# Optimization experiments

Measured on AMD Instinct MI355X. Metric: run time of the kernel, lower is better.

## Reference

```python
import jax, jax.numpy as jnp
import numpy as np

N_NODES = 50000
N_EDGES = 800000
IN_CH = 128
HID = 128
OUT_CH = 16
N_LAYERS = 3
N_GRAPHS = 128
BN_EPS = 1e-5


def setup_inputs() -> dict:
    key = jax.random.key(0)
    ks = jax.random.split(key, 12)
    x = jax.random.normal(ks[0], (N_NODES, IN_CH), dtype=jnp.float32)
    edge_index = jax.random.randint(ks[1], (2, N_EDGES), 0, N_NODES, dtype=jnp.int64)
    batch = jnp.sort(jax.random.randint(ks[2], (N_NODES,), 0, N_GRAPHS, dtype=jnp.int64))
    s = 1.0 / np.sqrt(HID)
    W1 = jax.random.normal(ks[3], (N_LAYERS, IN_CH, HID), dtype=jnp.float32) * s
    b1 = jax.random.normal(ks[4], (N_LAYERS, HID), dtype=jnp.float32) * s
    W2 = jax.random.normal(ks[5], (N_LAYERS, HID, HID), dtype=jnp.float32) * s
    b2 = jax.random.normal(ks[6], (N_LAYERS, HID), dtype=jnp.float32) * s
    gamma = jnp.ones((N_LAYERS, HID), dtype=jnp.float32)
    beta = jnp.zeros((N_LAYERS, HID), dtype=jnp.float32)
    mean = jax.random.normal(ks[7], (N_LAYERS, HID), dtype=jnp.float32) * 0.1
    var = jax.random.uniform(ks[8], (N_LAYERS, HID), dtype=jnp.float32, minval=0.5, maxval=1.5)
    Wc = jax.random.normal(ks[9], (HID, OUT_CH), dtype=jnp.float32) * s
    bc = jax.random.normal(ks[10], (OUT_CH,), dtype=jnp.float32) * s
    return {"x": x, "edge_index": edge_index, "batch": batch, "W1": W1, "b1": b1,
            "W2": W2, "b2": b2, "gamma": gamma, "beta": beta, "mean": mean,
            "var": var, "Wc": Wc, "bc": bc}


def reference(x, edge_index, batch, W1, b1, W2, b2, gamma, beta, mean, var, Wc, bc):
    # GIN (eval mode: BN uses running stats, dropout is identity).
    src, dst = edge_index[0], edge_index[1]
    n = x.shape[0]
    h = x
    for i in range(N_LAYERS):
        # GINConv with eps=0: MLP(x + sum_{j->i} x_j)
        agg = jax.ops.segment_sum(h[src], dst, num_segments=n)  # [N, d]
        z = h + agg
        z = jnp.maximum(z @ W1[i] + b1[i], 0.0) @ W2[i] + b2[i]  # 2-layer MLP
        # BatchNorm1d (eval) + ReLU
        inv = gamma[i] * jax.lax.rsqrt(var[i] + BN_EPS)
        h = jnp.maximum((z - mean[i]) * inv + beta[i], 0.0)
    pooled = jax.ops.segment_sum(h, batch, num_segments=N_GRAPHS)  # [G, hid]
    return pooled @ Wc + bc
```

## Files before the change

### kernel.cpp

```cpp
#include <hip/hip_runtime.h>

#define N_NODES 50000
#define N_EDGES 800000
#define CH 128
#define N_GRAPHS 128
#define N_LAYERS 3
#define OUT_CH 16
#define BN_EPS 1e-5f
#define ZN N_NODES
#define NB 196
#define BCAP 4608
#define PBCAP 8448
#define EPB 4096
#define NTILES (N_NODES / 16)
#define SSTRIDE 20
#define BINB 196
#define CB 6250
#define PB 388

typedef unsigned short ushort_t;
typedef __attribute__((ext_vector_type(8))) short bf16x8;
typedef __attribute__((ext_vector_type(8))) unsigned short u16x8;
typedef __attribute__((ext_vector_type(4))) float f32x4;

__device__ inline ushort_t f2b(float f) {
    unsigned u = __float_as_uint(f);
    unsigned r = (u + 0x7fffu + ((u >> 16) & 1u)) >> 16;
    return (ushort_t)r;
}
__device__ inline float blo(unsigned u) { return __uint_as_float(u << 16); }
__device__ inline float bhi(unsigned u) { return __uint_as_float(u & 0xffff0000u); }

__global__ __launch_bounds__(256) void setup_bin_kernel(
    const int* __restrict__ src, const int* __restrict__ dst,
    int* __restrict__ gcur, unsigned* __restrict__ gbuck,
    const float4* __restrict__ x, ushort4* __restrict__ xb, ushort4* __restrict__ xz,
    float* __restrict__ pooled,
    const float* __restrict__ W1, const float* __restrict__ W2, ushort_t* __restrict__ Wt,
    const float* __restrict__ b1, const float* __restrict__ b2,
    const float* __restrict__ gamma, const float* __restrict__ beta,
    const float* __restrict__ mean, const float* __restrict__ var,
    float* __restrict__ scale, float* __restrict__ shift) {
    int bid = blockIdx.x, t = threadIdx.x;
    if (bid < BINB) {
        __shared__ int lcnt[256];
        __shared__ int lpref[256];
        __shared__ int lpos[NB];
        __shared__ int lbase[NB];
        __shared__ unsigned stage[EPB];
        __shared__ unsigned char sbk[EPB];
        int e0 = bid * EPB;
        int nloc = N_EDGES - e0; if (nloc > EPB) nloc = EPB;

        lcnt[t] = 0;
        __syncthreads();

        int2 ed[16];
        const int4* s4 = (const int4*)(src + e0);
        const int4* d4 = (const int4*)(dst + e0);
        #pragma unroll
        for (int k = 0; k < 4; ++k) {
            int base = k * 1024 + t * 4;
            if (base + 3 < nloc) {
                int4 sv = s4[k * 256 + t];
                int4 dv = d4[k * 256 + t];
                ed[k * 4 + 0].x = sv.x; ed[k * 4 + 0].y = dv.x;
                ed[k * 4 + 1].x = sv.y; ed[k * 4 + 1].y = dv.y;
                ed[k * 4 + 2].x = sv.z; ed[k * 4 + 2].y = dv.z;
                ed[k * 4 + 3].x = sv.w; ed[k * 4 + 3].y = dv.w;
            } else {
                #pragma unroll
                for (int m = 0; m < 4; ++m) {
                    int i = base + m;
                    if (i < nloc) {
                        ed[k * 4 + m].x = src[e0 + i];
                        ed[k * 4 + m].y = dst[e0 + i];
                    } else ed[k * 4 + m].y = -1;
                }
            }
        }
        #pragma unroll
        for (int j = 0; j < 16; ++j)
            if (ed[j].y >= 0) atomicAdd(&lcnt[ed[j].y >> 8], 1);
        __syncthreads();
        int v = lcnt[t];
        lpref[t] = v;
        __syncthreads();
        for (int off = 1; off < 256; off <<= 1) {
            int y = (t >= off) ? lpref[t - off] : 0;
            __syncthreads();
            lpref[t] += y;
            __syncthreads();
        }
        int excl = lpref[t] - v;
        __syncthreads();
        lpref[t] = excl;
        if (t < NB) {
            lpos[t] = excl;
            lbase[t] = atomicAdd(&gcur[t], v);
        }
        __syncthreads();
        #pragma unroll
        for (int j = 0; j < 16; ++j) {
            if (ed[j].y >= 0) {
                int b = ed[j].y >> 8;
                int slot = atomicAdd(&lpos[b], 1);
                stage[slot] = (unsigned)ed[j].x | ((unsigned)(ed[j].y & 255) << 16);
                sbk[slot] = (unsigned char)b;
            }
        }
        __syncthreads();
        for (int i = t; i < nloc; i += 256) {
            int b = sbk[i];
            gbuck[(size_t)b * BCAP + lbase[b] + (i - lpref[b])] = stage[i];
        }
    } else if (bid < BINB + CB) {
        int i = (bid - BINB) * 256 + t;
        if (i < N_GRAPHS * CH) pooled[i] = 0.f;
        if (bid == BINB && t < 32) {
            ushort4 zz; zz.x = 0; zz.y = 0; zz.z = 0; zz.w = 0;
            xb[(size_t)ZN * 32 + t] = zz;
            xz[(size_t)ZN * 32 + t] = zz;
        }
        float4 v = x[i];
        ushort4 o;
        o.x = f2b(v.x); o.y = f2b(v.y); o.z = f2b(v.z); o.w = f2b(v.w);
        xb[i] = o;
    } else {
        int i = (bid - BINB - CB) * 256 + t;
        if (i < 6 * CH * CH) {
            int mat = i >> 14, r = i & 16383;
            int j = r & 7, bb = r >> 3;
            int lane = bb & 63, cs = bb >> 6;
            int ct = cs >> 2, ks = cs & 3;
            int n = ct * 16 + (lane & 15);
            int k = ks * 32 + (lane >> 4) * 8 + j;
            const float* Wsrc = (mat < 3) ? (W1 + (size_t)mat * CH * CH)
                                          : (W2 + (size_t)(mat - 3) * CH * CH);
            Wt[i] = f2b(Wsrc[k * CH + n]);
        } else {
            int e = i - 6 * CH * CH;
            if (e >= 6 * CH) return;
            int mat = e / CH, c = e % CH;
            if (mat < 3) {
                scale[e] = 1.f;
                shift[e] = b1[mat * CH + c];
            } else {
                int l = mat - 3;
                float inv = gamma[l * CH + c] * rsqrtf(var[l * CH + c] + BN_EPS);
                scale[e] = inv;
                shift[e] = (b2[l * CH + c] - mean[l * CH + c]) * inv + beta[l * CH + c];
            }
        }
    }
}

__global__ __launch_bounds__(256) void place_kernel(const int* __restrict__ gcur,
                                                    const unsigned* __restrict__ gbuck,
                                                    int* __restrict__ rowptr,
                                                    ushort_t* __restrict__ esrc) {
    __shared__ ushort_t ssrc[BCAP];
    __shared__ unsigned char sd[BCAP];
    __shared__ ushort_t outS[PBCAP];
    __shared__ int cnt[256], pref[256], cur[256];
    int b = blockIdx.x, t = threadIdx.x;
    cnt[t] = 0;
    __syncthreads();
    int nb = gcur[b];
    for (int i = t; i < nb; i += 256) {
        unsigned p = gbuck[(size_t)b * BCAP + i];
        ssrc[i] = (ushort_t)(p & 0xffffu);
        int dl = (p >> 16) & 0xff;
        sd[i] = (unsigned char)dl;
        atomicAdd(&cnt[dl], 1);
    }
    __syncthreads();
    int v = cnt[t];
    int pc = (v + 15) & ~15;
    pref[t] = pc;
    __syncthreads();
    for (int off = 1; off < 256; off <<= 1) {
        int y = (t >= off) ? pref[t - off] : 0;
        __syncthreads();
        pref[t] += y;
        __syncthreads();
    }
    int excl = pref[t] - pc;
    int total = pref[255];
    __syncthreads();
    pref[t] = excl;
    cur[t] = 0;
    int idx = (b << 8) + t;
    if (idx < N_NODES)
        rowptr[idx] = (b * PBCAP + excl) | ((pc >> 4) << 24);
    __syncthreads();
    for (int i = t; i < total; i += 256) outS[i] = (ushort_t)ZN;
    __syncthreads();
    for (int i = t; i < nb; i += 256) {
        int dl = sd[i];
        int p = pref[dl] + atomicAdd(&cur[dl], 1);
        outS[p] = ssrc[i];
    }
    __syncthreads();
    for (int i = t; i < total; i += 256)
        esrc[(size_t)b * PBCAP + i] = outS[i];
}

__global__ __launch_bounds__(512, 8) void layer_kernel(
    const unsigned* __restrict__ h2, const int* __restrict__ rowptr,
    const ushort_t* __restrict__ esrc,
    const ushort_t* __restrict__ Wf1, const ushort_t* __restrict__ Wf2,
    const float* __restrict__ shift1, const float* __restrict__ scale2,
    const float* __restrict__ shift2, ushort_t* __restrict__ hout,
    const int* __restrict__ batch, float* __restrict__ pooled, int do_pool) {
    __shared__ unsigned zt[16][68];
    __shared__ ushort_t sS[CH * SSTRIDE];

    int t = threadIdx.x;
    int wave = t >> 6, lane = t & 63;
    int quad = lane >> 4, l16 = lane & 15;
    int row0 = blockIdx.x * 16;

    {
        int node0 = row0 + wave * 2;
        unsigned self0 = h2[(size_t)node0 * 64 + lane];
        unsigned self1 = h2[(size_t)(node0 + 1) * 64 + lane];
        int pr0 = __builtin_amdgcn_readfirstlane(rowptr[node0]);
        int pr1 = __builtin_amdgcn_readfirstlane(rowptr[node0 + 1]);
        int e  = pr0 & 0xFFFFFF;
        int rA = (int)((unsigned)pr0 >> 24);
        int rounds = rA + (int)((unsigned)pr1 >> 24);
        float ax = blo(self0), ay = bhi(self0);
        float sx = 0.f, sy = 0.f;
        unsigned ucur[16];
        if (rounds > 0) {
            u16x8 i0 = *(const u16x8*)(esrc + e);
            u16x8 i1 = *(const u16x8*)(esrc + e + 8);
            #pragma unroll
            for (int j = 0; j < 8; ++j) ucur[j] = h2[(size_t)i0[j] * 64 + lane];
            #pragma unroll
            for (int j = 0; j < 8; ++j) ucur[8 + j] = h2[(size_t)i1[j] * 64 + lane];
        }
        for (int r = 0; r < rounds; ++r) {
            unsigned un[16];
            if (r + 1 < rounds) {
                const ushort_t* ep = esrc + e + 16;
                u16x8 i0 = *(const u16x8*)ep;
                u16x8 i1 = *(const u16x8*)(ep + 8);
                #pragma unroll
                for (int j = 0; j < 8; ++j) un[j] = h2[(size_t)i0[j] * 64 + lane];
                #pragma unroll
                for (int j = 0; j < 8; ++j) un[8 + j] = h2[(size_t)i1[j] * 64 + lane];
            }
            if (r == rA) { sx = ax; sy = ay; ax = blo(self1); ay = bhi(self1); }
            #pragma unroll
            for (int j = 0; j < 16; ++j) { ax += blo(ucur[j]); ay += bhi(ucur[j]); }
            if (r + 1 < rounds) {
                #pragma unroll
                for (int j = 0; j < 16; ++j) ucur[j] = un[j];
            }
            e += 16;
        }
        float bx, by;
        if (rA == rounds) {
            sx = ax; sy = ay;
            bx = blo(self1); by = bhi(self1);
        } else {
            bx = ax; by = ay;
        }
        zt[wave * 2][lane]     = ((unsigned)f2b(sy) << 16) | (unsigned)f2b(sx);
        zt[wave * 2 + 1][lane] = ((unsigned)f2b(by) << 16) | (unsigned)f2b(bx);
    }
    __syncthreads();

    {
        bf16x8 af[4];
        #pragma unroll
        for (int ks = 0; ks < 4; ++ks)
            af[ks] = *(const bf16x8*)((const ushort_t*)&zt[l16][0] + ks * 32 + quad * 8);
        bf16x8 w1[4];
        #pragma unroll
        for (int ks = 0; ks < 4; ++ks)
            w1[ks] = *(const bf16x8*)(Wf1 + ((size_t)(wave * 4 + ks) * 64 + lane) * 8);
        f32x4 acc = (f32x4){0.f, 0.f, 0.f, 0.f};
        #pragma unroll
        for (int ks = 0; ks < 4; ++ks)
            acc = __builtin_amdgcn_mfma_f32_16x16x32_bf16(af[ks], w1[ks], acc, 0, 0, 0);
        int k = wave * 16 + l16;
        float sh = shift1[k];
        uint2 p;
        p.x = ((unsigned)f2b(fmaxf(acc[1] + sh, 0.f)) << 16)
            |  (unsigned)f2b(fmaxf(acc[0] + sh, 0.f));
        p.y = ((unsigned)f2b(fmaxf(acc[3] + sh, 0.f)) << 16)
            |  (unsigned)f2b(fmaxf(acc[2] + sh, 0.f));
        *(uint2*)&sS[k * SSTRIDE + quad * 4] = p;
    }
    __syncthreads();

    {
        bf16x8 af2[4];
        #pragma unroll
        for (int ks = 0; ks < 4; ++ks)
            #pragma unroll
            for (int j = 0; j < 8; ++j)
                af2[ks][j] = (short)sS[(ks * 32 + quad * 8 + j) * SSTRIDE + l16];
        bf16x8 w2[4];
        #pragma unroll
        for (int ks = 0; ks < 4; ++ks)
            w2[ks] = *(const bf16x8*)(Wf2 + ((size_t)(wave * 4 + ks) * 64 + lane) * 8);
        f32x4 acc = (f32x4){0.f, 0.f, 0.f, 0.f};
        #pragma unroll
        for (int ks = 0; ks < 4; ++ks)
            acc = __builtin_amdgcn_mfma_f32_16x16x32_bf16(af2[ks], w2[ks], acc, 0, 0, 0);
        int col = wave * 16 + l16;
        float sc = scale2[col], sh = shift2[col];
        float hv[4];
        #pragma unroll
        for (int r = 0; r < 4; ++r)
            hv[r] = fmaxf(acc[r] * sc + sh, 0.f);
        if (!do_pool) {
            #pragma unroll
            for (int r = 0; r < 4; ++r) {
                int row = row0 + quad * 4 + r;
                hout[(size_t)row * CH + col] = f2b(hv[r]);
            }
        } else {
            int g0 = batch[row0], g15 = batch[row0 + 15];
            if (g0 == g15) {
                float s = hv[0] + hv[1] + hv[2] + hv[3];
                s += __shfl_xor(s, 16);
                s += __shfl_xor(s, 32);
                if (quad == 0) atomicAdd(&pooled[g0 * CH + col], s);
            } else {
                #pragma unroll
                for (int r = 0; r < 4; ++r) {
                    int row = row0 + quad * 4 + r;
                    atomicAdd(&pooled[batch[row] * CH + col], hv[r]);
                }
            }
        }
    }
}

__global__ __launch_bounds__(256) void cls_kernel(const float* __restrict__ pooled,
                                                  const float* __restrict__ Wc,
                                                  const float* __restrict__ bc,
                                                  float* __restrict__ out) {
    int i = blockIdx.x * blockDim.x + threadIdx.x;
    if (i >= N_GRAPHS * OUT_CH) return;
    int g = i / OUT_CH, o = i % OUT_CH;
    float s = bc[o];
    for (int k = 0; k < CH; ++k) s += pooled[g * CH + k] * Wc[k * OUT_CH + o];
    out[i] = s;
}

extern "C" void kernel_launch(void* const* d_in, const int* in_sizes, int n_in,
                              void* d_out, int out_size, void* d_ws, size_t ws_size,
                              hipStream_t stream) {
    const float* x     = (const float*)d_in[0];
    const int*   eidx  = (const int*)d_in[1];
    const int*   batch = (const int*)d_in[2];
    const float* W1    = (const float*)d_in[3];
    const float* b1    = (const float*)d_in[4];
    const float* W2    = (const float*)d_in[5];
    const float* b2    = (const float*)d_in[6];
    const float* gamma = (const float*)d_in[7];
    const float* beta  = (const float*)d_in[8];
    const float* mean  = (const float*)d_in[9];
    const float* var   = (const float*)d_in[10];
    const float* Wc    = (const float*)d_in[11];
    const float* bc    = (const float*)d_in[12];
    float* out = (float*)d_out;

    const int* src = eidx;
    const int* dst = eidx + N_EDGES;

    char* w = (char*)d_ws;
    size_t off = 0;
    auto alloc = [&](size_t bytes) { void* p = w + off; off += (bytes + 255) & ~(size_t)255; return p; };
    int*      gcur   = (int*)alloc(NB * 4);
    unsigned* gbuck  = (unsigned*)alloc((size_t)NB * BCAP * 4);
    int*      rowptr = (int*)alloc(N_NODES * 4);
    ushort_t* esrc   = (ushort_t*)alloc((size_t)NB * PBCAP * 2);
    ushort_t* Bh     = (ushort_t*)alloc((size_t)(N_NODES + 1) * CH * 2);
    ushort_t* Bz     = (ushort_t*)alloc((size_t)(N_NODES + 1) * CH * 2);
    ushort_t* Wt     = (ushort_t*)alloc((size_t)6 * CH * CH * 2);
    float*    scale  = (float*)alloc(6 * CH * 4);
    float*    shift  = (float*)alloc(6 * CH * 4);
    float*    pooled = (float*)alloc(N_GRAPHS * CH * 4);
    (void)ws_size; (void)n_in; (void)in_sizes; (void)out_size;

    hipMemsetAsync(gcur, 0, NB * 4, stream);
    setup_bin_kernel<<<BINB + CB + PB, 256, 0, stream>>>(
        src, dst, gcur, gbuck,
        (const float4*)x, (ushort4*)Bh, (ushort4*)Bz, pooled,
        W1, W2, Wt, b1, b2, gamma, beta, mean, var, scale, shift);
    place_kernel<<<NB, 256, 0, stream>>>(gcur, gbuck, rowptr, esrc);

    ushort_t* bufA = Bh;
    ushort_t* bufB = Bz;
    for (int i = 0; i < N_LAYERS; ++i) {
        int last = (i == N_LAYERS - 1);
        layer_kernel<<<NTILES, 512, 0, stream>>>((const unsigned*)bufA, rowptr, esrc,
                                                 Wt + (size_t)i * CH * CH,
                                                 Wt + (size_t)(3 + i) * CH * CH,
                                                 shift + i * CH,
                                                 scale + (3 + i) * CH,
                                                 shift + (3 + i) * CH,
                                                 bufB, batch, pooled, last);
        ushort_t* tmp = bufA; bufA = bufB; bufB = tmp;
    }

    cls_kernel<<<(N_GRAPHS * OUT_CH + 255) / 256, 256, 0, stream>>>(pooled, Wc, bc, out);
}
```

Baseline: 261.7 us.

## Balance neighbor aggregation across waves via 16-edge chunks with LDS atomics

Replaces the per-wave two-node aggregation loop with a block-wide loop over padded 16-edge chunks, striding chunks across the 8 waves. A new chunk-to-node map built in place_kernel tells each chunk which local row to add into, and partial sums are accumulated with float atomics in an LDS tile initialised with the self features. This is meant to remove load imbalance between waves caused by varying node degrees, at the cost of LDS atomics, an extra barrier, loss of the software-pipelined prefetch, and per-element bf16 packing when reading the A fragments.

```diff
diff --git a/kernel.cpp b/kernel.cpp
--- a/kernel.cpp
+++ b/kernel.cpp
@@ -11,6 +11,7 @@
 #define NB 196
 #define BCAP 4608
 #define PBCAP 8448
+#define NCHK (PBCAP / 16)
 #define EPB 4096
 #define NTILES (N_NODES / 16)
 #define SSTRIDE 20
@@ -158,10 +159,12 @@
 __global__ __launch_bounds__(256) void place_kernel(const int* __restrict__ gcur,
                                                     const unsigned* __restrict__ gbuck,
                                                     int* __restrict__ rowptr,
-                                                    ushort_t* __restrict__ esrc) {
+                                                    ushort_t* __restrict__ esrc,
+                                                    unsigned char* __restrict__ cnode) {
     __shared__ ushort_t ssrc[BCAP];
     __shared__ unsigned char sd[BCAP];
     __shared__ ushort_t outS[PBCAP];
+    __shared__ unsigned char cnodeS[NCHK];
     __shared__ int cnt[256], pref[256], cur[256];
     int b = blockIdx.x, t = threadIdx.x;
     cnt[t] = 0;
@@ -193,6 +196,7 @@
     int idx = (b << 8) + t;
     if (idx < N_NODES)
         rowptr[idx] = (b * PBCAP + excl) | ((pc >> 4) << 24);
+    for (int c = excl >> 4; c < (excl + pc) >> 4; ++c) cnodeS[c] = (unsigned char)t;
     __syncthreads();
     for (int i = t; i < total; i += 256) outS[i] = (ushort_t)ZN;
     __syncthreads();
@@ -204,16 +208,18 @@
     __syncthreads();
     for (int i = t; i < total; i += 256)
         esrc[(size_t)b * PBCAP + i] = outS[i];
+    for (int i = t; i < (total >> 4); i += 256)
+        cnode[b * NCHK + i] = cnodeS[i];
 }
 
 __global__ __launch_bounds__(512, 8) void layer_kernel(
     const unsigned* __restrict__ h2, const int* __restrict__ rowptr,
-    const ushort_t* __restrict__ esrc,
+    const ushort_t* __restrict__ esrc, const unsigned char* __restrict__ cnode,
     const ushort_t* __restrict__ Wf1, const ushort_t* __restrict__ Wf2,
     const float* __restrict__ shift1, const float* __restrict__ scale2,
     const float* __restrict__ shift2, ushort_t* __restrict__ hout,
     const int* __restrict__ batch, float* __restrict__ pooled, int do_pool) {
-    __shared__ unsigned zt[16][68];
+    __shared__ float ztf[16][2][66];
     __shared__ ushort_t sS[CH * SSTRIDE];
 
     int t = threadIdx.x;
@@ -225,51 +231,31 @@
         int node0 = row0 + wave * 2;
         unsigned self0 = h2[(size_t)node0 * 64 + lane];
         unsigned self1 = h2[(size_t)(node0 + 1) * 64 + lane];
-        int pr0 = __builtin_amdgcn_readfirstlane(rowptr[node0]);
-        int pr1 = __builtin_amdgcn_readfirstlane(rowptr[node0 + 1]);
-        int e  = pr0 & 0xFFFFFF;
-        int rA = (int)((unsigned)pr0 >> 24);
-        int rounds = rA + (int)((unsigned)pr1 >> 24);
-        float ax = blo(self0), ay = bhi(self0);
-        float sx = 0.f, sy = 0.f;
-        unsigned ucur[16];
-        if (rounds > 0) {
-            u16x8 i0 = *(const u16x8*)(esrc + e);
-            u16x8 i1 = *(const u16x8*)(esrc + e + 8);
-            #pragma unroll
-            for (int j = 0; j < 8; ++j) ucur[j] = h2[(size_t)i0[j] * 64 + lane];
-            #pragma unroll
-            for (int j = 0; j < 8; ++j) ucur[8 + j] = h2[(size_t)i1[j] * 64 + lane];
-        }
-        for (int r = 0; r < rounds; ++r) {
-            unsigned un[16];
-            if (r + 1 < rounds) {
-                const ushort_t* ep = esrc + e + 16;
-                u16x8 i0 = *(const u16x8*)ep;
-                u16x8 i1 = *(const u16x8*)(ep + 8);
-                #pragma unroll
-                for (int j = 0; j < 8; ++j) un[j] = h2[(size_t)i0[j] * 64 + lane];
-                #pragma unroll
-                for (int j = 0; j < 8; ++j) un[8 + j] = h2[(size_t)i1[j] * 64 + lane];
-            }
-            if (r == rA) { sx = ax; sy = ay; ax = blo(self1); ay = bhi(self1); }
-            #pragma unroll
-            for (int j = 0; j < 16; ++j) { ax += blo(ucur[j]); ay += bhi(ucur[j]); }
-            if (r + 1 < rounds) {
-                #pragma unroll
-                for (int j = 0; j < 16; ++j) ucur[j] = un[j];
-            }
-            e += 16;
-        }
-        float bx, by;
-        if (rA == rounds) {
-            sx = ax; sy = ay;
-            bx = blo(self1); by = bhi(self1);
-        } else {
-            bx = ax; by = ay;
-        }
-        zt[wave * 2][lane]     = ((unsigned)f2b(sy) << 16) | (unsigned)f2b(sx);
-        zt[wave * 2 + 1][lane] = ((unsigned)f2b(by) << 16) | (unsigned)f2b(bx);
+        ztf[wave * 2][0][lane]     = blo(self0);
+        ztf[wave * 2][1][lane]     = bhi(self0);
+        ztf[wave * 2 + 1][0][lane] = blo(self1);
+        ztf[wave * 2 + 1][1][lane] = bhi(self1);
+        int pr0 = __builtin_amdgcn_readfirstlane(rowptr[row0]);
+        int prF = __builtin_amdgcn_readfirstlane(rowptr[row0 + 15]);
+        int c0 = (pr0 & 0xFFFFFF) >> 4;
+        int c1 = ((prF & 0xFFFFFF) >> 4) + (int)((unsigned)prF >> 24);
+        __syncthreads();
+        for (int c = c0 + wave; c < c1; c += 8) {
+            const ushort_t* ep = esrc + ((size_t)c << 4);
+            u16x8 i0 = *(const u16x8*)ep;
+            u16x8 i1 = *(const u16x8*)(ep + 8);
+            unsigned u[16];
+            #pragma unroll
+            for (int j = 0; j < 8; ++j) u[j] = h2[(size_t)i0[j] * 64 + lane];
+            #pragma unroll
+            for (int j = 0; j < 8; ++j) u[8 + j] = h2[(size_t)i1[j] * 64 + lane];
+            float ax = 0.f, ay = 0.f;
+            #pragma unroll
+            for (int j = 0; j < 16; ++j) { ax += blo(u[j]); ay += bhi(u[j]); }
+            int li = cnode[c] & 15;
+            atomicAdd(&ztf[li][0][lane], ax);
+            atomicAdd(&ztf[li][1][lane], ay);
+        }
     }
     __syncthreads();
 
@@ -277,7 +263,11 @@
         bf16x8 af[4];
         #pragma unroll
         for (int ks = 0; ks < 4; ++ks)
-            af[ks] = *(const bf16x8*)((const ushort_t*)&zt[l16][0] + ks * 32 + quad * 8);
+            #pragma unroll
+            for (int j = 0; j < 8; ++j) {
+                int ch = ks * 32 + quad * 8 + j;
+                af[ks][j] = (short)f2b(ztf[l16][ch & 1][ch >> 1]);
+            }
         bf16x8 w1[4];
         #pragma unroll
         for (int ks = 0; ks < 4; ++ks)
@@ -382,6 +372,7 @@
     unsigned* gbuck  = (unsigned*)alloc((size_t)NB * BCAP * 4);
     int*      rowptr = (int*)alloc(N_NODES * 4);
     ushort_t* esrc   = (ushort_t*)alloc((size_t)NB * PBCAP * 2);
+    unsigned char* cnode = (unsigned char*)alloc((size_t)NB * NCHK);
     ushort_t* Bh     = (ushort_t*)alloc((size_t)(N_NODES + 1) * CH * 2);
     ushort_t* Bz     = (ushort_t*)alloc((size_t)(N_NODES + 1) * CH * 2);
     ushort_t* Wt     = (ushort_t*)alloc((size_t)6 * CH * CH * 2);
@@ -395,13 +386,13 @@
         src, dst, gcur, gbuck,
         (const float4*)x, (ushort4*)Bh, (ushort4*)Bz, pooled,
         W1, W2, Wt, b1, b2, gamma, beta, mean, var, scale, shift);
-    place_kernel<<<NB, 256, 0, stream>>>(gcur, gbuck, rowptr, esrc);
+    place_kernel<<<NB, 256, 0, stream>>>(gcur, gbuck, rowptr, esrc, cnode);
 
     ushort_t* bufA = Bh;
     ushort_t* bufB = Bz;
     for (int i = 0; i < N_LAYERS; ++i) {
         int last = (i == N_LAYERS - 1);
-        layer_kernel<<<NTILES, 512, 0, stream>>>((const unsigned*)bufA, rowptr, esrc,
+        layer_kernel<<<NTILES, 512, 0, stream>>>((const unsigned*)bufA, rowptr, esrc, cnode,
                                                  Wt + (size_t)i * CH * CH,
                                                  Wt + (size_t)(3 + i) * CH * CH,
                                                  shift + i * CH,
```

Result: slower. 319.1 us (+21.9%).

## Balance per-wave aggregation by pairing heaviest and lightest nodes in each tile

Applied to the files above, without the earlier changes.

The bucketing pass now also sorts the 16 nodes of every tile by their padded neighbour-round count and stores that order. Each wave in the layer kernel then aggregates the k-th heaviest and k-th lightest node of its tile, so per-wave work is more even than with consecutive node pairs. The aggregation loop also drops the register double-buffered prefetch of the next 16 neighbour rows for a simpler per-round gather, which may expose more load latency. It adds a small serial insertion sort in the place kernel and one extra byte lookup per wave.

```diff
diff --git a/kernel.cpp b/kernel.cpp
--- a/kernel.cpp
+++ b/kernel.cpp
@@ -158,10 +158,12 @@
 __global__ __launch_bounds__(256) void place_kernel(const int* __restrict__ gcur,
                                                     const unsigned* __restrict__ gbuck,
                                                     int* __restrict__ rowptr,
-                                                    ushort_t* __restrict__ esrc) {
+                                                    ushort_t* __restrict__ esrc,
+                                                    unsigned char* __restrict__ nodeord) {
     __shared__ ushort_t ssrc[BCAP];
     __shared__ unsigned char sd[BCAP];
     __shared__ ushort_t outS[PBCAP];
+    __shared__ unsigned char rndS[256];
     __shared__ int cnt[256], pref[256], cur[256];
     int b = blockIdx.x, t = threadIdx.x;
     cnt[t] = 0;
@@ -190,11 +192,28 @@
     __syncthreads();
     pref[t] = excl;
     cur[t] = 0;
+    rndS[t] = (unsigned char)(pc >> 4);
     int idx = (b << 8) + t;
     if (idx < N_NODES)
         rowptr[idx] = (b * PBCAP + excl) | ((pc >> 4) << 24);
     __syncthreads();
     for (int i = t; i < total; i += 256) outS[i] = (ushort_t)ZN;
+    if (t < 16) {
+        int base = t << 4;
+        unsigned char ids[16];
+        #pragma unroll
+        for (int i = 0; i < 16; ++i) ids[i] = (unsigned char)i;
+        for (int i = 1; i < 16; ++i) {
+            unsigned char id = ids[i];
+            int key = rndS[base + id];
+            int j = i - 1;
+            while (j >= 0 && (int)rndS[base + ids[j]] < key) { ids[j + 1] = ids[j]; --j; }
+            ids[j + 1] = id;
+        }
+        #pragma unroll
+        for (int i = 0; i < 16; ++i)
+            nodeord[(b << 8) + base + i] = ids[i];
+    }
     __syncthreads();
     for (int i = t; i < nb; i += 256) {
         int dl = sd[i];
@@ -208,7 +227,7 @@
 
 __global__ __launch_bounds__(512, 8) void layer_kernel(
     const unsigned* __restrict__ h2, const int* __restrict__ rowptr,
-    const ushort_t* __restrict__ esrc,
+    const ushort_t* __restrict__ esrc, const unsigned char* __restrict__ nodeord,
     const ushort_t* __restrict__ Wf1, const ushort_t* __restrict__ Wf2,
     const float* __restrict__ shift1, const float* __restrict__ scale2,
     const float* __restrict__ shift2, ushort_t* __restrict__ hout,
@@ -222,54 +241,32 @@
     int row0 = blockIdx.x * 16;
 
     {
-        int node0 = row0 + wave * 2;
-        unsigned self0 = h2[(size_t)node0 * 64 + lane];
-        unsigned self1 = h2[(size_t)(node0 + 1) * 64 + lane];
-        int pr0 = __builtin_amdgcn_readfirstlane(rowptr[node0]);
-        int pr1 = __builtin_amdgcn_readfirstlane(rowptr[node0 + 1]);
-        int e  = pr0 & 0xFFFFFF;
-        int rA = (int)((unsigned)pr0 >> 24);
-        int rounds = rA + (int)((unsigned)pr1 >> 24);
-        float ax = blo(self0), ay = bhi(self0);
-        float sx = 0.f, sy = 0.f;
-        unsigned ucur[16];
-        if (rounds > 0) {
-            u16x8 i0 = *(const u16x8*)(esrc + e);
-            u16x8 i1 = *(const u16x8*)(esrc + e + 8);
-            #pragma unroll
-            for (int j = 0; j < 8; ++j) ucur[j] = h2[(size_t)i0[j] * 64 + lane];
-            #pragma unroll
-            for (int j = 0; j < 8; ++j) ucur[8 + j] = h2[(size_t)i1[j] * 64 + lane];
-        }
-        for (int r = 0; r < rounds; ++r) {
-            unsigned un[16];
-            if (r + 1 < rounds) {
-                const ushort_t* ep = esrc + e + 16;
-                u16x8 i0 = *(const u16x8*)ep;
-                u16x8 i1 = *(const u16x8*)(ep + 8);
+        int oa = __builtin_amdgcn_readfirstlane(nodeord[row0 + wave]);
+        int ob = __builtin_amdgcn_readfirstlane(nodeord[row0 + 15 - wave]);
+        #pragma unroll
+        for (int nn = 0; nn < 2; ++nn) {
+            int lo = (nn == 0) ? oa : ob;
+            int node = row0 + lo;
+            unsigned self = h2[(size_t)node * 64 + lane];
+            float ax = blo(self), ay = bhi(self);
+            int pr = __builtin_amdgcn_readfirstlane(rowptr[node]);
+            int e = pr & 0xFFFFFF;
+            int rounds = (int)((unsigned)pr >> 24);
+            for (int r = 0; r < rounds; ++r, e += 16) {
+                u16x8 i0 = *(const u16x8*)(esrc + e);
+                u16x8 i1 = *(const u16x8*)(esrc + e + 8);
+                unsigned u[16];
                 #pragma unroll
-                for (int j = 0; j < 8; ++j) un[j] = h2[(size_t)i0[j] * 64 + lane];
+                for (int j = 0; j < 8; ++j)
+                    u[j] = h2[(size_t)i0[j] * 64 + lane];
                 #pragma unroll
-                for (int j = 0; j < 8; ++j) un[8 + j] = h2[(size_t)i1[j] * 64 + lane];
-            }
-            if (r == rA) { sx = ax; sy = ay; ax = blo(self1); ay = bhi(self1); }
-            #pragma unroll
-            for (int j = 0; j < 16; ++j) { ax += blo(ucur[j]); ay += bhi(ucur[j]); }
-            if (r + 1 < rounds) {
+                for (int j = 0; j < 8; ++j)
+                    u[8 + j] = h2[(size_t)i1[j] * 64 + lane];
                 #pragma unroll
-                for (int j = 0; j < 16; ++j) ucur[j] = un[j];
-            }
-            e += 16;
-        }
-        float bx, by;
-        if (rA == rounds) {
-            sx = ax; sy = ay;
-            bx = blo(self1); by = bhi(self1);
-        } else {
-            bx = ax; by = ay;
-        }
-        zt[wave * 2][lane]     = ((unsigned)f2b(sy) << 16) | (unsigned)f2b(sx);
-        zt[wave * 2 + 1][lane] = ((unsigned)f2b(by) << 16) | (unsigned)f2b(bx);
+                for (int j = 0; j < 16; ++j) { ax += blo(u[j]); ay += bhi(u[j]); }
+            }
+            zt[lo][lane] = ((unsigned)f2b(ay) << 16) | (unsigned)f2b(ax);
+        }
     }
     __syncthreads();
 
@@ -382,6 +379,7 @@
     unsigned* gbuck  = (unsigned*)alloc((size_t)NB * BCAP * 4);
     int*      rowptr = (int*)alloc(N_NODES * 4);
     ushort_t* esrc   = (ushort_t*)alloc((size_t)NB * PBCAP * 2);
+    unsigned char* nodeord = (unsigned char*)alloc((size_t)NB * 256);
     ushort_t* Bh     = (ushort_t*)alloc((size_t)(N_NODES + 1) * CH * 2);
     ushort_t* Bz     = (ushort_t*)alloc((size_t)(N_NODES + 1) * CH * 2);
     ushort_t* Wt     = (ushort_t*)alloc((size_t)6 * CH * CH * 2);
@@ -395,13 +393,13 @@
         src, dst, gcur, gbuck,
         (const float4*)x, (ushort4*)Bh, (ushort4*)Bz, pooled,
         W1, W2, Wt, b1, b2, gamma, beta, mean, var, scale, shift);
-    place_kernel<<<NB, 256, 0, stream>>>(gcur, gbuck, rowptr, esrc);
+    place_kernel<<<NB, 256, 0, stream>>>(gcur, gbuck, rowptr, esrc, nodeord);
 
     ushort_t* bufA = Bh;
     ushort_t* bufB = Bz;
     for (int i = 0; i < N_LAYERS; ++i) {
         int last = (i == N_LAYERS - 1);
-        layer_kernel<<<NTILES, 512, 0, stream>>>((const unsigned*)bufA, rowptr, esrc,
+        layer_kernel<<<NTILES, 512, 0, stream>>>((const unsigned*)bufA, rowptr, esrc, nodeord,
                                                  Wt + (size_t)i * CH * CH,
                                                  Wt + (size_t)(3 + i) * CH * CH,
                                                  shift + i * CH,
```

After: 221.1 us. -15.5%, faster.
